# Performance work log

Measured on AMD Instinct MI355X. Metric: run time of the kernel, lower is better.

The kernel has to match this reference:

```python
import jax, jax.numpy as jnp
import numpy as np

N = 50000

def gcn_conv(h, W, b, src, dst, n):
    # h: [N, Fin] -> linear transform then normalized scatter-add aggregation
    h = h @ W  # [N, Fout]
    # add self-loops (PyG GCNConv default)
    loop = jnp.arange(n, dtype=src.dtype)
    s = jnp.concatenate([src, loop])
    d = jnp.concatenate([dst, loop])
    # symmetric normalization: deg^{-1/2}[s] * deg^{-1/2}[d], deg over target index
    deg = jax.ops.segment_sum(jnp.ones_like(d, dtype=h.dtype), d, num_segments=n)
    dinv = jnp.where(deg > 0, jax.lax.rsqrt(deg), 0.0)
    norm = dinv[s] * dinv[d]  # [E+N]
    msg = h[s] * norm[:, None]  # gather + scale
    out = jax.ops.segment_sum(msg, d, num_segments=n)  # scatter-add
    return out + b


def setup_inputs() -> dict:
    key = jax.random.key(0)
    k1, k2, k3, k4, k5, k6 = jax.random.split(key, 6)
    Fin, Fh, Fout = 512, 256, 64
    E = 800000
    x = jax.random.normal(k1, (N, Fin), dtype=jnp.float32)
    edge_index = jax.random.randint(k2, (2, E), 0, N, dtype=jnp.int64)
    # Glorot-style init matching nn Parameter scale
    W1 = jax.random.normal(k3, (Fin, Fh), dtype=jnp.float32) * (1.0 / np.sqrt(Fin))
    b1 = jnp.zeros((Fh,), dtype=jnp.float32)
    W2 = jax.random.normal(k4, (Fh, Fout), dtype=jnp.float32) * (1.0 / np.sqrt(Fh))
    b2 = jnp.zeros((Fout,), dtype=jnp.float32)
    return {"x": x, "edge_index": edge_index, "W1": W1, "b1": b1, "W2": W2, "b2": b2}


def reference(x, edge_index, W1, b1, W2, b2):
    src, dst = edge_index[0], edge_index[1]
    h1 = jax.nn.relu(gcn_conv(x, W1, b1, src, dst, N))
    # dropout is identity in eval mode
    h2 = gcn_conv(h1, W2, b2, src, dst, N)
    return jax.nn.log_softmax(h2, axis=1)
```

## Files before the change

kernel.cpp:

```cpp
#include <hip/hip_runtime.h>
#include <hip/hip_bf16.h>

typedef __attribute__((ext_vector_type(8))) short short8;
typedef __attribute__((ext_vector_type(4))) float f32x4;

#define NNODES 50000

#define VM_BAR() asm volatile("s_waitcnt vmcnt(0)\n\ts_barrier" ::: "memory")

__device__ __forceinline__ float b2f(unsigned short s) {
  union { unsigned int u; float f; } c; c.u = ((unsigned int)s) << 16;
  return c.f;
}
__device__ __forceinline__ unsigned short f2b(float f) {
  return __bfloat16_as_ushort(__float2bfloat16(f));
}
__device__ __forceinline__ unsigned int pkcvt(float a, float b) {
  return (unsigned int)f2b(a) | ((unsigned int)f2b(b) << 16);
}

__device__ __forceinline__ void gl_lds16(const void* g, void* l) {
  __builtin_amdgcn_global_load_lds((const __attribute__((address_space(1))) unsigned int*)g,
                                   (__attribute__((address_space(3))) unsigned int*)l, 16, 0, 0);
}

__global__ __launch_bounds__(256) void k_deg(const int* __restrict__ ei, int* __restrict__ deg, int E,
                                             const float* __restrict__ W1, const float* __restrict__ W2,
                                             unsigned short* __restrict__ w1t, unsigned short* __restrict__ w2t,
                                             const float* __restrict__ x, unsigned short* __restrict__ xb) {
  int idx = blockIdx.x * 256 + threadIdx.x;
  if (idx < E) atomicAdd(&deg[ei[E + idx]], 1);
  if (idx < 256 * 512) { int nn = idx >> 9, kk = idx & 511; w1t[idx] = f2b(W1[kk * 256 + nn]); }
  int i2 = idx - 256 * 512;
  if (i2 >= 0 && i2 < 64 * 256) { int nn = i2 >> 8, kk = i2 & 255; w2t[i2] = f2b(W2[kk * 64 + nn]); }
  if (idx < (NNODES * 512) / 8) {
    const float4 v0 = *(const float4*)(x + (size_t)idx * 8);
    const float4 v1 = *(const float4*)(x + (size_t)idx * 8 + 4);
    uint4 p;
    p.x = pkcvt(v0.x, v0.y); p.y = pkcvt(v0.z, v0.w);
    p.z = pkcvt(v1.x, v1.y); p.w = pkcvt(v1.z, v1.w);
    *(uint4*)(xb + (size_t)idx * 8) = p;
  }
}

__global__ __launch_bounds__(256) void k_scanA(const int* __restrict__ deg, int* __restrict__ excl,
                                               int* __restrict__ blksum, float* __restrict__ dinv, int n) {
  const int i = blockIdx.x * 256 + threadIdx.x;
  const int lane = threadIdx.x & 63, wid = threadIdx.x >> 6;
  const int v = (i < n) ? deg[i] : 0;
  int x = v;
#pragma unroll
  for (int o = 1; o < 64; o <<= 1) {
    int y = __shfl_up(x, o, 64);
    if (lane >= o) x += y;
  }
  __shared__ int wsum[4];
  if (lane == 63) wsum[wid] = x;
  __syncthreads();
  int woff = 0;
  for (int w = 0; w < wid; ++w) woff += wsum[w];
  const int incl = x + woff;
  if (i < n) {
    excl[i] = incl - v;
    dinv[i] = rsqrtf((float)v + 1.0f);
  }
  if (threadIdx.x == 255) blksum[blockIdx.x] = incl;
}

__global__ __launch_bounds__(256) void k_scanC(const int* __restrict__ excl, const int* __restrict__ blksum,
                                               int* __restrict__ rowptr, int* __restrict__ cursor, int n, int E) {
  const int t = threadIdx.x;
  int partial = 0;
  for (int j = t; j < (int)blockIdx.x; j += 256) partial += blksum[j];
#pragma unroll
  for (int o = 32; o > 0; o >>= 1) partial += __shfl_xor(partial, o, 64);
  __shared__ int ws[4];
  if ((t & 63) == 0) ws[t >> 6] = partial;
  __syncthreads();
  const int off = ws[0] + ws[1] + ws[2] + ws[3];
  const int i = blockIdx.x * 256 + t;
  if (i < n) {
    int r = excl[i] + off;
    rowptr[i] = r;
    cursor[i] = r;
  }
  if (i == 0) rowptr[n] = E;
}

__global__ __launch_bounds__(256) void k_fill(const int* __restrict__ ei, int* __restrict__ cursor,
                                              int* __restrict__ csr, int E) {
  int e = blockIdx.x * 256 + threadIdx.x;
  if (e < E) {
    int pos = atomicAdd(&cursor[ei[E + e]], 1);
    csr[pos] = ei[e];
  }
}

__global__ __launch_bounds__(256) void k_gemm1(const unsigned short* __restrict__ xb,
    const unsigned short* __restrict__ w1t, const float* __restrict__ dinv,
    unsigned short* __restrict__ hs1b) {
  const int M = NNODES, K = 512, N = 256;
  const int NRB = (NNODES + 127) / 128;
  const int bid = blockIdx.x;
  const int rowblk = (bid >> 5) * 8 + (bid & 7);
  const int colblk = (bid >> 3) & 3;
  if (rowblk >= NRB) return;

  __shared__ unsigned short Ab[2][128][32];
  __shared__ unsigned short Bb[2][64][32];

  const int tid = threadIdx.x;
  const int w = tid >> 6, lane = tid & 63;
  const int sub = lane >> 2, c = lane & 3;
  const int brow = rowblk * 128, bcol = colblk * 64;
  const int wr = w >> 1, wc = w & 1;
  const int lr = lane & 15, lk = lane >> 4;

  int gr0 = brow + w * 16 + sub;      if (gr0 >= M) gr0 = M - 1;
  int gr1 = brow + 64 + w * 16 + sub; if (gr1 >= M) gr1 = M - 1;
  const int grB = bcol + w * 16 + sub;

  const unsigned short* a0p = xb + (size_t)gr0 * K + c * 8;
  const unsigned short* a1p = xb + (size_t)gr1 * K + c * 8;
  const unsigned short* bp  = w1t + (size_t)grB * K + c * 8;

  f32x4 acc[4][2] = {};

#define G1_STAGE(BUF, KT) do { \
    gl_lds16(a0p + (KT), &Ab[BUF][w * 16][0]); \
    gl_lds16(a1p + (KT), &Ab[BUF][64 + w * 16][0]); \
    gl_lds16(bp  + (KT), &Bb[BUF][w * 16][0]); \
  } while (0)

  G1_STAGE(0, 0);
  VM_BAR();

  for (int s = 0; s < 16; ++s) {
    const int cur = s & 1;
    if (s < 15) G1_STAGE(cur ^ 1, (s + 1) * 32);
    short8 af[4], bf[2];
#pragma unroll
    for (int m = 0; m < 4; ++m) af[m] = *(const short8*)&Ab[cur][wr * 64 + m * 16 + lr][lk * 8];
#pragma unroll
    for (int n = 0; n < 2; ++n) bf[n] = *(const short8*)&Bb[cur][wc * 32 + n * 16 + lr][lk * 8];
#pragma unroll
    for (int m = 0; m < 4; ++m)
#pragma unroll
      for (int n = 0; n < 2; ++n)
        acc[m][n] = __builtin_amdgcn_mfma_f32_16x16x32_bf16(af[m], bf[n], acc[m][n], 0, 0, 0);
    VM_BAR();
  }
#undef G1_STAGE

#pragma unroll
  for (int m = 0; m < 4; ++m) {
#pragma unroll
    for (int n = 0; n < 2; ++n) {
      const int col = bcol + wc * 32 + n * 16 + lr;
#pragma unroll
      for (int j = 0; j < 4; ++j) {
        const int row = brow + wr * 64 + m * 16 + lk * 4 + j;
        if (row < M) hs1b[(size_t)row * N + col] = f2b(acc[m][n][j] * dinv[row]);
      }
    }
  }
}

__global__ __launch_bounds__(256) void k_agg1g(const int* __restrict__ rowptr,
    const int* __restrict__ csr, const unsigned short* __restrict__ hs1b,
    const float* __restrict__ dinv, const float* __restrict__ b1,
    const unsigned short* __restrict__ w2t, unsigned short* __restrict__ hs2b) {
  const int M = NNODES;
  __shared__ unsigned short h1t[16][264];
  const int tid = threadIdx.x;
  const int w = tid >> 6, lane = tid & 63;
  const int lr = lane & 15, lk = lane >> 4;
  const int brow = blockIdx.x * 16;

  const float4 bb = *(const float4*)(b1 + lane * 4);

  for (int i = 0; i < 4; ++i) {
    const int ldsrow = w * 4 + i;
    const int d = brow + ldsrow;
    f32x4 acc = {0.f, 0.f, 0.f, 0.f};
    if (d < M) {
      const int a = rowptr[d], bnd = rowptr[d + 1];
      ushort4 sv = *(const ushort4*)(hs1b + (size_t)d * 256 + lane * 4);
      acc[0] = b2f(sv.x); acc[1] = b2f(sv.y); acc[2] = b2f(sv.z); acc[3] = b2f(sv.w);
      int e = a;
      for (; e + 8 <= bnd; e += 8) {
        int s[8];
#pragma unroll
        for (int j = 0; j < 8; ++j) s[j] = csr[e + j];
        ushort4 v[8];
#pragma unroll
        for (int j = 0; j < 8; ++j) v[j] = *(const ushort4*)(hs1b + (size_t)s[j] * 256 + lane * 4);
#pragma unroll
        for (int j = 0; j < 8; ++j) {
          acc[0] += b2f(v[j].x); acc[1] += b2f(v[j].y);
          acc[2] += b2f(v[j].z); acc[3] += b2f(v[j].w);
        }
      }
      for (; e + 2 <= bnd; e += 2) {
        int s0 = csr[e], s1 = csr[e + 1];
        ushort4 v0 = *(const ushort4*)(hs1b + (size_t)s0 * 256 + lane * 4);
        ushort4 v1 = *(const ushort4*)(hs1b + (size_t)s1 * 256 + lane * 4);
        acc[0] += b2f(v0.x) + b2f(v1.x); acc[1] += b2f(v0.y) + b2f(v1.y);
        acc[2] += b2f(v0.z) + b2f(v1.z); acc[3] += b2f(v0.w) + b2f(v1.w);
      }
      for (; e < bnd; ++e) {
        int s0 = csr[e];
        ushort4 v0 = *(const ushort4*)(hs1b + (size_t)s0 * 256 + lane * 4);
        acc[0] += b2f(v0.x); acc[1] += b2f(v0.y); acc[2] += b2f(v0.z); acc[3] += b2f(v0.w);
      }
      const float di = dinv[d];
      acc[0] = fmaxf(0.f, acc[0] * di + bb.x);
      acc[1] = fmaxf(0.f, acc[1] * di + bb.y);
      acc[2] = fmaxf(0.f, acc[2] * di + bb.z);
      acc[3] = fmaxf(0.f, acc[3] * di + bb.w);
    }
    uint2 pk;
    pk.x = pkcvt(acc[0], acc[1]);
    pk.y = pkcvt(acc[2], acc[3]);
    *(uint2*)&h1t[ldsrow][lane * 4] = pk;
  }

  __syncthreads();

  f32x4 acc2 = {};
#pragma unroll
  for (int s = 0; s < 8; ++s) {
    short8 af = *(const short8*)&h1t[lr][s * 32 + lk * 8];
    short8 bfv = *(const short8*)(w2t + (size_t)(w * 16 + lr) * 256 + s * 32 + lk * 8);
    acc2 = __builtin_amdgcn_mfma_f32_16x16x32_bf16(af, bfv, acc2, 0, 0, 0);
  }

  {
    const int col = w * 16 + lr;
#pragma unroll
    for (int j = 0; j < 4; ++j) {
      const int row = brow + lk * 4 + j;
      if (row < M) hs2b[(size_t)row * 64 + col] = f2b(acc2[j] * dinv[row]);
    }
  }
}

__global__ __launch_bounds__(256) void k_agg2f(const int* __restrict__ rowptr,
    const int* __restrict__ csr, const unsigned short* __restrict__ hs2b,
    const float* __restrict__ dinv, const float* __restrict__ b2,
    float* __restrict__ out) {
  const int d = blockIdx.x * 4 + (threadIdx.x >> 6);
  if (d >= NNODES) return;
  const int lane = threadIdx.x & 63;
  const int a = rowptr[d], bnd = rowptr[d + 1];

  float acc = b2f(hs2b[(size_t)d * 64 + lane]);

  int i = a;
  for (; i + 8 <= bnd; i += 8) {
    int s[8];
#pragma unroll
    for (int j = 0; j < 8; ++j) s[j] = csr[i + j];
    unsigned short v[8];
#pragma unroll
    for (int j = 0; j < 8; ++j) v[j] = hs2b[(size_t)s[j] * 64 + lane];
#pragma unroll
    for (int j = 0; j < 8; ++j) acc += b2f(v[j]);
  }
  for (; i < bnd; ++i) acc += b2f(hs2b[(size_t)csr[i] * 64 + lane]);

  float v = acc * dinv[d] + b2[lane];
  float m = v;
#pragma unroll
  for (int o = 32; o > 0; o >>= 1) m = fmaxf(m, __shfl_xor(m, o, 64));
  float ex = expf(v - m);
  float s = ex;
#pragma unroll
  for (int o = 32; o > 0; o >>= 1) s += __shfl_xor(s, o, 64);
  out[(size_t)d * 64 + lane] = v - m - logf(s);
}

extern "C" void kernel_launch(void* const* d_in, const int* in_sizes, int n_in,
                              void* d_out, int out_size, void* d_ws, size_t ws_size,
                              hipStream_t stream) {
  const float* x  = (const float*)d_in[0];
  const int*   ei = (const int*)d_in[1];
  const float* W1 = (const float*)d_in[2];
  const float* b1 = (const float*)d_in[3];
  const float* W2 = (const float*)d_in[4];
  const float* b2 = (const float*)d_in[5];
  float* out = (float*)d_out;
  const int E = in_sizes[1] / 2;
  const int n = NNODES;
  const int nblk = (n + 255) / 256;

  char* ws = (char*)d_ws;
  size_t off = 0;
  auto alloc = [&](size_t bytes) { char* p = ws + off; off = (off + bytes + 255) & ~(size_t)255; return p; };
  int*            deg    = (int*)alloc((size_t)n * 4);
  float*          dinv   = (float*)alloc((size_t)n * 4);
  int*            excl   = (int*)alloc((size_t)n * 4);
  int*            blksum = (int*)alloc((size_t)nblk * 4);
  int*            rowptr = (int*)alloc((size_t)(n + 1) * 4);
  int*            cursor = (int*)alloc((size_t)n * 4);
  int*            csr    = (int*)alloc((size_t)E * 4);
  unsigned short* w1t    = (unsigned short*)alloc(256 * 512 * 2);
  unsigned short* w2t    = (unsigned short*)alloc(64 * 256 * 2);
  unsigned short* hs1b   = (unsigned short*)alloc((size_t)n * 256 * 2);
  unsigned short* hs2b   = (unsigned short*)alloc((size_t)n * 64 * 2);
  unsigned short* xb     = (unsigned short*)alloc((size_t)n * 512 * 2);
  (void)ws_size; (void)n_in; (void)out_size;

  hipMemsetAsync(deg, 0, (size_t)n * 4, stream);
  k_deg<<<(NNODES * 512 / 8 + 255) / 256, 256, 0, stream>>>(ei, deg, E, W1, W2, w1t, w2t, x, xb);
  k_scanA<<<nblk, 256, 0, stream>>>(deg, excl, blksum, dinv, n);
  k_scanC<<<nblk, 256, 0, stream>>>(excl, blksum, rowptr, cursor, n, E);
  k_fill<<<(E + 255) / 256, 256, 0, stream>>>(ei, cursor, csr, E);
  k_gemm1<<<49 * 32, 256, 0, stream>>>(xb, w1t, dinv, hs1b);
  k_agg1g<<<(n + 15) / 16, 256, 0, stream>>>(rowptr, csr, hs1b, dinv, b1, w2t, hs2b);
  k_agg2f<<<(n + 3) / 4, 256, 0, stream>>>(rowptr, csr, hs2b, dinv, b2, out);
}
```

Before: 256.6 us.

## Split layer-1 features into column slices for aggregation and unfuse second GEMM

GEMM1 now writes its output as eight 32-column slices, each stored as [N,32]. A new aggregation kernel walks the CSR once per slice (block index mod 8), so each slice's gather working set is about 3.2 MB and should stay in cache. The layer-2 GEMM is split out into its own MFMA kernel that reads the sliced aggregated features through LDS double buffering. In exchange, the CSR indices are read eight times, a 25 MB intermediate round-trips through memory, and there is one extra launch.

```diff
diff --git a/kernel.cpp b/kernel.cpp
--- a/kernel.cpp
+++ b/kernel.cpp
@@ -3,6 +3,7 @@
 
 typedef __attribute__((ext_vector_type(8))) short short8;
 typedef __attribute__((ext_vector_type(4))) float f32x4;
+typedef __attribute__((ext_vector_type(2))) unsigned int uint2v;
 
 #define NNODES 50000
 
@@ -98,8 +99,8 @@
 
 __global__ __launch_bounds__(256) void k_gemm1(const unsigned short* __restrict__ xb,
     const unsigned short* __restrict__ w1t, const float* __restrict__ dinv,
-    unsigned short* __restrict__ hs1b) {
-  const int M = NNODES, K = 512, N = 256;
+    unsigned short* __restrict__ hs1cb) {
+  const int M = NNODES, K = 512;
   const int NRB = (NNODES + 127) / 128;
   const int bid = blockIdx.x;
   const int rowblk = (bid >> 5) * 8 + (bid & 7);
@@ -156,91 +157,113 @@
   for (int m = 0; m < 4; ++m) {
 #pragma unroll
     for (int n = 0; n < 2; ++n) {
-      const int col = bcol + wc * 32 + n * 16 + lr;
+      const int cb = colblk * 2 + wc;
+      const int cw = n * 16 + lr;
 #pragma unroll
       for (int j = 0; j < 4; ++j) {
         const int row = brow + wr * 64 + m * 16 + lk * 4 + j;
-        if (row < M) hs1b[(size_t)row * N + col] = f2b(acc[m][n][j] * dinv[row]);
+        if (row < M) hs1cb[((size_t)cb * NNODES + row) * 32 + cw] = f2b(acc[m][n][j] * dinv[row]);
       }
     }
   }
 }
 
-__global__ __launch_bounds__(256) void k_agg1g(const int* __restrict__ rowptr,
-    const int* __restrict__ csr, const unsigned short* __restrict__ hs1b,
+__global__ __launch_bounds__(256) void k_agg1(const int* __restrict__ rowptr,
+    const int* __restrict__ csr, const unsigned short* __restrict__ hs1cb,
     const float* __restrict__ dinv, const float* __restrict__ b1,
-    const unsigned short* __restrict__ w2t, unsigned short* __restrict__ hs2b) {
+    unsigned short* __restrict__ h1agg) {
+  const int p = blockIdx.x & 7;
+  const int chunk = blockIdx.x >> 3;
+  const int w = threadIdx.x >> 6, lane = threadIdx.x & 63;
+  const int g = lane >> 3, cs = lane & 7;
+  const int d = chunk * 32 + w * 8 + g;
+  if (d >= NNODES) return;
+  const unsigned short* __restrict__ slice = hs1cb + (size_t)p * (NNODES * 32);
+  const int a = rowptr[d], bnd = rowptr[d + 1];
+
+  ushort4 sv = *(const ushort4*)(slice + (size_t)d * 32 + cs * 4);
+  float a0 = b2f(sv.x), a1 = b2f(sv.y), a2 = b2f(sv.z), a3 = b2f(sv.w);
+
+  for (int e = a; __any(e < bnd); e += 4) {
+#pragma unroll
+    for (int k = 0; k < 4; ++k) {
+      if (e + k < bnd) {
+        const int s = __builtin_nontemporal_load(csr + e + k);
+        ushort4 v = *(const ushort4*)(slice + (size_t)s * 32 + cs * 4);
+        a0 += b2f(v.x); a1 += b2f(v.y); a2 += b2f(v.z); a3 += b2f(v.w);
+      }
+    }
+  }
+
+  const float di = dinv[d];
+  const float4 bb = *(const float4*)(b1 + p * 32 + cs * 4);
+  a0 = fmaxf(0.f, a0 * di + bb.x);
+  a1 = fmaxf(0.f, a1 * di + bb.y);
+  a2 = fmaxf(0.f, a2 * di + bb.z);
+  a3 = fmaxf(0.f, a3 * di + bb.w);
+  uint2v pk;
+  pk.x = pkcvt(a0, a1);
+  pk.y = pkcvt(a2, a3);
+  __builtin_nontemporal_store(pk, (uint2v*)(h1agg + (size_t)p * (NNODES * 32) + (size_t)d * 32 + cs * 4));
+}
+
+__global__ __launch_bounds__(256) void k_gemm2(const unsigned short* __restrict__ h1agg,
+    const unsigned short* __restrict__ w2t, const float* __restrict__ dinv,
+    unsigned short* __restrict__ hs2b) {
   const int M = NNODES;
-  __shared__ unsigned short h1t[16][264];
+  const size_t SL = (size_t)NNODES * 32;
+  const int brow = blockIdx.x * 64;
+
+  __shared__ unsigned short As[2][64][32];
+  __shared__ unsigned short Bs[2][64][32];
+
   const int tid = threadIdx.x;
   const int w = tid >> 6, lane = tid & 63;
+  const int sub = lane >> 2, c = lane & 3;
+  const int wr = w >> 1, wc = w & 1;
   const int lr = lane & 15, lk = lane >> 4;
-  const int brow = blockIdx.x * 16;
-
-  const float4 bb = *(const float4*)(b1 + lane * 4);
-
-  for (int i = 0; i < 4; ++i) {
-    const int ldsrow = w * 4 + i;
-    const int d = brow + ldsrow;
-    f32x4 acc = {0.f, 0.f, 0.f, 0.f};
-    if (d < M) {
-      const int a = rowptr[d], bnd = rowptr[d + 1];
-      ushort4 sv = *(const ushort4*)(hs1b + (size_t)d * 256 + lane * 4);
-      acc[0] = b2f(sv.x); acc[1] = b2f(sv.y); acc[2] = b2f(sv.z); acc[3] = b2f(sv.w);
-      int e = a;
-      for (; e + 8 <= bnd; e += 8) {
-        int s[8];
-#pragma unroll
-        for (int j = 0; j < 8; ++j) s[j] = csr[e + j];
-        ushort4 v[8];
-#pragma unroll
-        for (int j = 0; j < 8; ++j) v[j] = *(const ushort4*)(hs1b + (size_t)s[j] * 256 + lane * 4);
-#pragma unroll
-        for (int j = 0; j < 8; ++j) {
-          acc[0] += b2f(v[j].x); acc[1] += b2f(v[j].y);
-          acc[2] += b2f(v[j].z); acc[3] += b2f(v[j].w);
-        }
+
+  int gr = brow + w * 16 + sub; if (gr >= M) gr = M - 1;
+  const unsigned short* ap = h1agg + (size_t)gr * 32 + c * 8;
+  const unsigned short* bp = w2t + (size_t)(w * 16 + sub) * 256 + c * 8;
+
+  f32x4 acc[2][2] = {};
+
+#define G2_STAGE(BUF, S) do { \
+    gl_lds16(ap + (size_t)(S) * SL, &As[BUF][w * 16][0]); \
+    gl_lds16(bp + (S) * 32,         &Bs[BUF][w * 16][0]); \
+  } while (0)
+
+  G2_STAGE(0, 0);
+  VM_BAR();
+
+  for (int s = 0; s < 8; ++s) {
+    const int cur = s & 1;
+    if (s < 7) G2_STAGE(cur ^ 1, s + 1);
+    short8 af[2], bf[2];
+#pragma unroll
+    for (int m = 0; m < 2; ++m) af[m] = *(const short8*)&As[cur][wr * 32 + m * 16 + lr][lk * 8];
+#pragma unroll
+    for (int n = 0; n < 2; ++n) bf[n] = *(const short8*)&Bs[cur][wc * 32 + n * 16 + lr][lk * 8];
+#pragma unroll
+    for (int m = 0; m < 2; ++m)
+#pragma unroll
+      for (int n = 0; n < 2; ++n)
+        acc[m][n] = __builtin_amdgcn_mfma_f32_16x16x32_bf16(af[m], bf[n], acc[m][n], 0, 0, 0);
+    VM_BAR();
+  }
+#undef G2_STAGE
+
+#pragma unroll
+  for (int m = 0; m < 2; ++m) {
+#pragma unroll
+    for (int n = 0; n < 2; ++n) {
+      const int col = wc * 32 + n * 16 + lr;
+#pragma unroll
+      for (int j = 0; j < 4; ++j) {
+        const int row = brow + wr * 32 + m * 16 + lk * 4 + j;
+        if (row < M) hs2b[(size_t)row * 64 + col] = f2b(acc[m][n][j] * dinv[row]);
       }
-      for (; e + 2 <= bnd; e += 2) {
-        int s0 = csr[e], s1 = csr[e + 1];
-        ushort4 v0 = *(const ushort4*)(hs1b + (size_t)s0 * 256 + lane * 4);
-        ushort4 v1 = *(const ushort4*)(hs1b + (size_t)s1 * 256 + lane * 4);
-        acc[0] += b2f(v0.x) + b2f(v1.x); acc[1] += b2f(v0.y) + b2f(v1.y);
-        acc[2] += b2f(v0.z) + b2f(v1.z); acc[3] += b2f(v0.w) + b2f(v1.w);
-      }
-      for (; e < bnd; ++e) {
-        int s0 = csr[e];
-        ushort4 v0 = *(const ushort4*)(hs1b + (size_t)s0 * 256 + lane * 4);
-        acc[0] += b2f(v0.x); acc[1] += b2f(v0.y); acc[2] += b2f(v0.z); acc[3] += b2f(v0.w);
-      }
-      const float di = dinv[d];
-      acc[0] = fmaxf(0.f, acc[0] * di + bb.x);
-      acc[1] = fmaxf(0.f, acc[1] * di + bb.y);
-      acc[2] = fmaxf(0.f, acc[2] * di + bb.z);
-      acc[3] = fmaxf(0.f, acc[3] * di + bb.w);
-    }
-    uint2 pk;
-    pk.x = pkcvt(acc[0], acc[1]);
-    pk.y = pkcvt(acc[2], acc[3]);
-    *(uint2*)&h1t[ldsrow][lane * 4] = pk;
-  }
-
-  __syncthreads();
-
-  f32x4 acc2 = {};
-#pragma unroll
-  for (int s = 0; s < 8; ++s) {
-    short8 af = *(const short8*)&h1t[lr][s * 32 + lk * 8];
-    short8 bfv = *(const short8*)(w2t + (size_t)(w * 16 + lr) * 256 + s * 32 + lk * 8);
-    acc2 = __builtin_amdgcn_mfma_f32_16x16x32_bf16(af, bfv, acc2, 0, 0, 0);
-  }
-
-  {
-    const int col = w * 16 + lr;
-#pragma unroll
-    for (int j = 0; j < 4; ++j) {
-      const int row = brow + lk * 4 + j;
-      if (row < M) hs2b[(size_t)row * 64 + col] = f2b(acc2[j] * dinv[row]);
     }
   }
 }
@@ -306,7 +329,8 @@
   int*            csr    = (int*)alloc((size_t)E * 4);
   unsigned short* w1t    = (unsigned short*)alloc(256 * 512 * 2);
   unsigned short* w2t    = (unsigned short*)alloc(64 * 256 * 2);
-  unsigned short* hs1b   = (unsigned short*)alloc((size_t)n * 256 * 2);
+  unsigned short* hs1cb  = (unsigned short*)alloc((size_t)n * 256 * 2);
+  unsigned short* h1agg  = (unsigned short*)alloc((size_t)n * 256 * 2);
   unsigned short* hs2b   = (unsigned short*)alloc((size_t)n * 64 * 2);
   unsigned short* xb     = (unsigned short*)alloc((size_t)n * 512 * 2);
   (void)ws_size; (void)n_in; (void)out_size;
@@ -316,7 +340,8 @@
   k_scanA<<<nblk, 256, 0, stream>>>(deg, excl, blksum, dinv, n);
   k_scanC<<<nblk, 256, 0, stream>>>(excl, blksum, rowptr, cursor, n, E);
   k_fill<<<(E + 255) / 256, 256, 0, stream>>>(ei, cursor, csr, E);
-  k_gemm1<<<49 * 32, 256, 0, stream>>>(xb, w1t, dinv, hs1b);
-  k_agg1g<<<(n + 15) / 16, 256, 0, stream>>>(rowptr, csr, hs1b, dinv, b1, w2t, hs2b);
+  k_gemm1<<<49 * 32, 256, 0, stream>>>(xb, w1t, dinv, hs1cb);
+  k_agg1<<<1563 * 8, 256, 0, stream>>>(rowptr, csr, hs1cb, dinv, b1, h1agg);
+  k_gemm2<<<(n + 63) / 64, 256, 0, stream>>>(h1agg, w2t, dinv, hs2b);
   k_agg2f<<<(n + 3) / 4, 256, 0, stream>>>(rowptr, csr, hs2b, dinv, b2, out);
 }
```

Result: slower. 328.8 us (+28.1%).
